# Kernel tuning notes

Hardware: AMD Instinct MI355X
Metric: run time of the kernel (lower is better)

Reference implementation:

```python
import jax, jax.numpy as jnp
import numpy as np

B, S = 256, 512
V, E, H, O = 256, 128, 256, 128


def setup_inputs() -> dict:
    key = jax.random.key(0)
    ks = jax.random.split(key, 8)
    s_e = 1.0 / np.sqrt(H)
    return {
        "x": jax.random.randint(ks[0], (B, S), 0, V),
        "emb": jax.random.normal(ks[1], (V, E), dtype=jnp.float32),
        "W_ih": jax.random.uniform(ks[2], (4 * H, E), jnp.float32, -s_e, s_e),
        "W_hh": jax.random.uniform(ks[3], (4 * H, H), jnp.float32, -s_e, s_e),
        "b_ih": jax.random.uniform(ks[4], (4 * H,), jnp.float32, -s_e, s_e),
        "b_hh": jax.random.uniform(ks[5], (4 * H,), jnp.float32, -s_e, s_e),
        "W_out": jax.random.uniform(ks[6], (O, H), jnp.float32, -s_e, s_e),
        "b_out": jax.random.uniform(ks[7], (O,), jnp.float32, -s_e, s_e),
    }


def _lstm_last_h(xe, W_ih, W_hh, b_ih, b_hh):
    # xe: [B, S, E]. Precompute input contribution to all gates: [S, B, 4H]
    pre = jnp.einsum("bse,ge->sbg", xe, W_ih) + (b_ih + b_hh)
    Bn = xe.shape[0]
    h0 = jnp.zeros((Bn, H), xe.dtype)
    c0 = jnp.zeros((Bn, H), xe.dtype)

    def step(carry, p):
        h, c = carry
        gates = p + h @ W_hh.T  # [B, 4H]
        i, f, g, o = jnp.split(gates, 4, axis=-1)  # PyTorch gate order i,f,g,o
        i = jax.nn.sigmoid(i)
        f = jax.nn.sigmoid(f)
        g = jnp.tanh(g)
        o = jax.nn.sigmoid(o)
        c = f * c + i * g
        h = o * jnp.tanh(c)
        return (h, c), None

    (h, _), _ = jax.lax.scan(step, (h0, c0), pre)
    return h  # [B, H] == lstm output at last timestep


def reference(x, emb, W_ih, W_hh, b_ih, b_hh, W_out, b_out):
    xe = emb[x]  # [B, S, E] embedding lookup
    h_last = _lstm_last_h(xe, W_ih, W_hh, b_ih, b_hh)
    return h_last @ W_out.T + b_out  # [B, O]
```

## Files before the change

kernel.cpp:

```cpp
#include <hip/hip_runtime.h>


typedef _Float16 f16x8 __attribute__((ext_vector_type(8)));
typedef _Float16 f16x4 __attribute__((ext_vector_type(4)));
typedef float    f32x4 __attribute__((ext_vector_type(4)));

#define B_  256
#define S_  512
#define V_  256
#define E_  128
#define H_  256
#define O_  128

#define T_OFF     0u
#define HLAST_OFF (512u << 10)
#define WPK_OFF   (768u << 10)

__global__ void build_table(const float* __restrict__ emb,
                            const float* __restrict__ W_ih,
                            const float* __restrict__ b_ih,
                            const float* __restrict__ b_hh,
                            _Float16* __restrict__ T2h) {
    const int v   = blockIdx.x;
    const int tid = threadIdx.x;

    __shared__ float e[E_];
    if (tid < E_) e[tid] = emb[v * E_ + tid];
    __syncthreads();

    f16x4 tv;
#pragma unroll
    for (int t = 0; t < 4; ++t) {
        const int g = t * 256 + tid;
        const float4* wp = (const float4*)(W_ih + g * E_);
        float acc = 0.f;
#pragma unroll
        for (int i = 0; i < E_ / 4; ++i) {
            float4 w = wp[i];
            acc += w.x * e[4*i] + w.y * e[4*i+1] + w.z * e[4*i+2] + w.w * e[4*i+3];
        }
        tv[t] = (_Float16)(acc + b_ih[g] + b_hh[g]);
    }
    *(f16x4*)(T2h + ((size_t)v * 256 + tid) * 4) = tv;
}

__global__ void prepack(const float* __restrict__ W_hh,
                        _Float16* __restrict__ Wpk) {
    const int blk = blockIdx.x;
    const int ktS = blk >> 3;
    const int j   = blk & 7;
    const int kt  = 6 + ktS;
    const int tid = threadIdx.x;
    const int wv = tid >> 6, l = tid & 63, l15 = l & 15, quad = l >> 4;
    const int n  = j * 128 + wv * 16 + l15;
    const int k0 = kt * 32 + quad * 8;
    const float4* wp = (const float4*)(W_hh + (size_t)n * H_ + k0);
    float4 w0 = wp[0];
    float4 w1 = wp[1];
    f16x8 f = (f16x8){
        (_Float16)w0.x, (_Float16)w0.y, (_Float16)w0.z, (_Float16)w0.w,
        (_Float16)w1.x, (_Float16)w1.y, (_Float16)w1.z, (_Float16)w1.w};
    *(f16x8*)(Wpk + ((size_t)blk * 512 + tid) * 8) = f;
}

__device__ __forceinline__ float sig_fast(float x) {
    float t = __builtin_amdgcn_exp2f(-1.4426950408889634f * x);
    return __builtin_amdgcn_rcpf(1.f + t);
}
__device__ __forceinline__ float tanh_fast(float x) {
    x = fminf(fmaxf(x, -30.f), 30.f);
    float t = __builtin_amdgcn_exp2f(-2.8853900817779268f * x);
    return (1.f - t) * __builtin_amdgcn_rcpf(1.f + t);
}

#define HSTRIDE 272

__launch_bounds__(512, 2)
__global__ void lstm_persistent(const int* __restrict__ x,
                                const float* __restrict__ W_hh,
                                const _Float16* __restrict__ T2h,
                                const _Float16* __restrict__ Wpk,
                                float* __restrict__ hlast) {
    const int tid    = threadIdx.x;
    const int wv     = tid >> 6;
    const int l      = tid & 63;
    const int l15    = l & 15;
    const int quad   = l >> 4;
    const int stripe = blockIdx.x;
    const int uu     = wv * 16 + l15;

    __shared__ __align__(16) _Float16 wlds[8][8][2][512];
    __shared__ __align__(16) _Float16 hbuf[2][4][HSTRIDE];
    __shared__ __align__(16) _Float16 zbuf[256];

    if (tid < 128) ((int*)zbuf)[tid] = 0;

    f16x8 wreg[8][4];
#pragma unroll
    for (int j = 0; j < 8; ++j) {
        const float* wr = W_hh + (size_t)(j * 128 + uu) * H_ + quad * 8;
#pragma unroll
        for (int kt = 0; kt < 6; ++kt) {
            const float4* wp = (const float4*)(wr + kt * 32);
            float4 w0 = wp[0];
            float4 w1 = wp[1];
            f16x8 f = (f16x8){
                (_Float16)w0.x, (_Float16)w0.y, (_Float16)w0.z, (_Float16)w0.w,
                (_Float16)w1.x, (_Float16)w1.y, (_Float16)w1.z, (_Float16)w1.w};
            if (kt < 2)
                *(f16x8*)&wlds[wv][j][kt][(size_t)l * 8] = f;
            else
                wreg[j][kt - 2] = f;
        }
    }

    const int grow = stripe * 4 + quad;
    float c2[2] = {0.f, 0.f};

    int xv = x[(size_t)grow * S_];

    __syncthreads();

    for (int s = 0; s < S_; ++s) {
        f16x4 tcv[2];
        tcv[0] = *(const f16x4*)(T2h + ((size_t)xv * 256 + uu) * 4);
        tcv[1] = *(const f16x4*)(T2h + ((size_t)xv * 256 + uu + 128) * 4);
        if (s + 1 < S_) xv = x[(size_t)grow * S_ + s + 1];

        f32x4 acc[8];
#pragma unroll
        for (int j = 0; j < 8; ++j) acc[j] = (f32x4){0.f, 0.f, 0.f, 0.f};

        if (s > 0) {
            const _Float16* ha = ((l15 & 3) == 0)
                ? (&hbuf[(s - 1) & 1][l15 >> 2][0] + quad * 8)
                : (zbuf + quad * 8);

#pragma unroll
            for (int pass = 0; pass < 2; ++pass) {
                f16x8 wstr[4][2];
#pragma unroll
                for (int jj = 0; jj < 4; ++jj)
#pragma unroll
                    for (int ktS = 0; ktS < 2; ++ktS)
                        wstr[jj][ktS] = *(const f16x8*)(
                            Wpk + ((size_t)((ktS * 8 + pass * 4 + jj) * 512 + tid)) * 8);

#pragma unroll
                for (int kt = 0; kt < 8; ++kt) {
                    f16x8 a = *(const f16x8*)(ha + kt * 32);
                    if (kt < 2) {
#pragma unroll
                        for (int jj = 0; jj < 4; ++jj) {
                            f16x8 b = *(const f16x8*)
                                &wlds[wv][pass * 4 + jj][kt][(size_t)l * 8];
                            acc[pass * 4 + jj] =
                                __builtin_amdgcn_mfma_f32_16x16x32_f16(
                                    a, b, acc[pass * 4 + jj], 0, 0, 0);
                        }
                    } else if (kt < 6) {
#pragma unroll
                        for (int jj = 0; jj < 4; ++jj)
                            acc[pass * 4 + jj] =
                                __builtin_amdgcn_mfma_f32_16x16x32_f16(
                                    a, wreg[pass * 4 + jj][kt - 2],
                                    acc[pass * 4 + jj], 0, 0, 0);
                    } else {
#pragma unroll
                        for (int jj = 0; jj < 4; ++jj)
                            acc[pass * 4 + jj] =
                                __builtin_amdgcn_mfma_f32_16x16x32_f16(
                                    a, wstr[jj][kt - 6],
                                    acc[pass * 4 + jj], 0, 0, 0);
                    }
                }
            }
        }

        const bool last = (s == S_ - 1);
#pragma unroll
        for (int p = 0; p < 2; ++p) {
            float gi = sig_fast (acc[0 + p][0] + (float)tcv[p][0]);
            float gf = sig_fast (acc[2 + p][0] + (float)tcv[p][1]);
            float gg = tanh_fast(acc[4 + p][0] + (float)tcv[p][2]);
            float go = sig_fast (acc[6 + p][0] + (float)tcv[p][3]);
            float cc = gf * c2[p] + gi * gg;
            c2[p] = cc;
            float hv = go * tanh_fast(cc);
            if (!last) {
                hbuf[s & 1][quad][uu + p * 128] = (_Float16)hv;
            } else {
                hlast[(size_t)grow * H_ + uu + p * 128] = hv;
            }
        }

        __syncthreads();
    }
}

__global__ void out_kernel(const float* __restrict__ hlast,
                           const float* __restrict__ W_out,
                           const float* __restrict__ b_out,
                           float* __restrict__ out) {
    const int b = blockIdx.x;
    const int o = threadIdx.x;
    __shared__ float hl[H_];
    hl[o]       = hlast[b * H_ + o];
    hl[o + 128] = hlast[b * H_ + o + 128];
    __syncthreads();
    const float4* wp = (const float4*)(W_out + o * H_);
    float acc = 0.f;
#pragma unroll
    for (int i = 0; i < H_ / 4; ++i) {
        float4 w = wp[i];
        acc += w.x * hl[4*i] + w.y * hl[4*i+1] + w.z * hl[4*i+2] + w.w * hl[4*i+3];
    }
    out[b * O_ + o] = acc + b_out[o];
}

extern "C" void kernel_launch(void* const* d_in, const int* in_sizes, int n_in,
                              void* d_out, int out_size, void* d_ws, size_t ws_size,
                              hipStream_t stream) {
    const int*   x     = (const int*)  d_in[0];
    const float* emb   = (const float*)d_in[1];
    const float* W_ih  = (const float*)d_in[2];
    const float* W_hh  = (const float*)d_in[3];
    const float* b_ih  = (const float*)d_in[4];
    const float* b_hh  = (const float*)d_in[5];
    const float* W_out = (const float*)d_in[6];
    const float* b_out = (const float*)d_in[7];
    float* out = (float*)d_out;

    char* ws = (char*)d_ws;
    _Float16* T2h   = (_Float16*)(ws + T_OFF);
    float*    hlast = (float*)(ws + HLAST_OFF);
    _Float16* Wpk   = (_Float16*)(ws + WPK_OFF);

    build_table<<<dim3(V_), dim3(256), 0, stream>>>(emb, W_ih, b_ih, b_hh, T2h);
    prepack<<<dim3(16), dim3(512), 0, stream>>>(W_hh, Wpk);
    lstm_persistent<<<dim3(64), dim3(512), 0, stream>>>(x, W_hh, T2h, Wpk, hlast);
    out_kernel<<<dim3(B_), dim3(O_), 0, stream>>>(hlast, W_out, b_out, out);
}
```

Measured before the change: 915.8 us.

## Split LSTM recurrence across 16 waves with one hidden-unit slice each

Doubles the persistent LSTM block from 512 to 1024 threads, so each wave computes the four gates for a single 16-unit slice instead of two. This halves the serial MFMA chain per wave on each time step. The W_hh split is rebalanced to two k-tiles in LDS, three in registers and three streamed from a repacked global buffer, with the streamed loads issued early inside the k-loop. The launch bound of (1024, 4) asks for more occupancy than a CU can hold and may tightly cap registers, which risks spills.

Result: slower. 1.162 ms (+26.9%).

```diff
diff --git a/kernel.cpp b/kernel.cpp
--- a/kernel.cpp
+++ b/kernel.cpp
@@ -47,12 +47,12 @@
 __global__ void prepack(const float* __restrict__ W_hh,
                         _Float16* __restrict__ Wpk) {
     const int blk = blockIdx.x;
-    const int ktS = blk >> 3;
-    const int j   = blk & 7;
-    const int kt  = 6 + ktS;
+    const int ktS = blk >> 2;
+    const int j   = blk & 3;
+    const int kt  = 5 + ktS;
     const int tid = threadIdx.x;
     const int wv = tid >> 6, l = tid & 63, l15 = l & 15, quad = l >> 4;
-    const int n  = j * 128 + wv * 16 + l15;
+    const int n  = j * 256 + wv * 16 + l15;
     const int k0 = kt * 32 + quad * 8;
     const float4* wp = (const float4*)(W_hh + (size_t)n * H_ + k0);
     float4 w0 = wp[0];
@@ -60,7 +60,7 @@
     f16x8 f = (f16x8){
         (_Float16)w0.x, (_Float16)w0.y, (_Float16)w0.z, (_Float16)w0.w,
         (_Float16)w1.x, (_Float16)w1.y, (_Float16)w1.z, (_Float16)w1.w};
-    *(f16x8*)(Wpk + ((size_t)blk * 512 + tid) * 8) = f;
+    *(f16x8*)(Wpk + ((size_t)blk * 1024 + tid) * 8) = f;
 }
 
 __device__ __forceinline__ float sig_fast(float x) {
@@ -75,7 +75,7 @@
 
 #define HSTRIDE 272
 
-__launch_bounds__(512, 2)
+__launch_bounds__(1024, 4)
 __global__ void lstm_persistent(const int* __restrict__ x,
                                 const float* __restrict__ W_hh,
                                 const _Float16* __restrict__ T2h,
@@ -89,18 +89,18 @@
     const int stripe = blockIdx.x;
     const int uu     = wv * 16 + l15;
 
-    __shared__ __align__(16) _Float16 wlds[8][8][2][512];
+    __shared__ __align__(16) _Float16 wlds[16][4][2][512];
     __shared__ __align__(16) _Float16 hbuf[2][4][HSTRIDE];
     __shared__ __align__(16) _Float16 zbuf[256];
 
     if (tid < 128) ((int*)zbuf)[tid] = 0;
 
-    f16x8 wreg[8][4];
-#pragma unroll
-    for (int j = 0; j < 8; ++j) {
-        const float* wr = W_hh + (size_t)(j * 128 + uu) * H_ + quad * 8;
-#pragma unroll
-        for (int kt = 0; kt < 6; ++kt) {
+    f16x8 wreg[4][3];
+#pragma unroll
+    for (int j = 0; j < 4; ++j) {
+        const float* wr = W_hh + (size_t)(j * 256 + uu) * H_ + quad * 8;
+#pragma unroll
+        for (int kt = 0; kt < 5; ++kt) {
             const float4* wp = (const float4*)(wr + kt * 32);
             float4 w0 = wp[0];
             float4 w1 = wp[1];
@@ -115,82 +115,89 @@
     }
 
     const int grow = stripe * 4 + quad;
-    float c2[2] = {0.f, 0.f};
+    float c1 = 0.f;
 
     int xv = x[(size_t)grow * S_];
 
     __syncthreads();
 
     for (int s = 0; s < S_; ++s) {
-        f16x4 tcv[2];
-        tcv[0] = *(const f16x4*)(T2h + ((size_t)xv * 256 + uu) * 4);
-        tcv[1] = *(const f16x4*)(T2h + ((size_t)xv * 256 + uu + 128) * 4);
+        f16x4 tcv = *(const f16x4*)(T2h + ((size_t)xv * 256 + uu) * 4);
         if (s + 1 < S_) xv = x[(size_t)grow * S_ + s + 1];
 
-        f32x4 acc[8];
-#pragma unroll
-        for (int j = 0; j < 8; ++j) acc[j] = (f32x4){0.f, 0.f, 0.f, 0.f};
+        f32x4 acc[4];
+#pragma unroll
+        for (int j = 0; j < 4; ++j) acc[j] = (f32x4){0.f, 0.f, 0.f, 0.f};
 
         if (s > 0) {
             const _Float16* ha = ((l15 & 3) == 0)
                 ? (&hbuf[(s - 1) & 1][l15 >> 2][0] + quad * 8)
                 : (zbuf + quad * 8);
 
-#pragma unroll
-            for (int pass = 0; pass < 2; ++pass) {
-                f16x8 wstr[4][2];
-#pragma unroll
-                for (int jj = 0; jj < 4; ++jj)
-#pragma unroll
-                    for (int ktS = 0; ktS < 2; ++ktS)
-                        wstr[jj][ktS] = *(const f16x8*)(
-                            Wpk + ((size_t)((ktS * 8 + pass * 4 + jj) * 512 + tid)) * 8);
-
-#pragma unroll
-                for (int kt = 0; kt < 8; ++kt) {
-                    f16x8 a = *(const f16x8*)(ha + kt * 32);
-                    if (kt < 2) {
-#pragma unroll
-                        for (int jj = 0; jj < 4; ++jj) {
-                            f16x8 b = *(const f16x8*)
-                                &wlds[wv][pass * 4 + jj][kt][(size_t)l * 8];
-                            acc[pass * 4 + jj] =
-                                __builtin_amdgcn_mfma_f32_16x16x32_f16(
-                                    a, b, acc[pass * 4 + jj], 0, 0, 0);
-                        }
-                    } else if (kt < 6) {
-#pragma unroll
-                        for (int jj = 0; jj < 4; ++jj)
-                            acc[pass * 4 + jj] =
-                                __builtin_amdgcn_mfma_f32_16x16x32_f16(
-                                    a, wreg[pass * 4 + jj][kt - 2],
-                                    acc[pass * 4 + jj], 0, 0, 0);
-                    } else {
-#pragma unroll
-                        for (int jj = 0; jj < 4; ++jj)
-                            acc[pass * 4 + jj] =
-                                __builtin_amdgcn_mfma_f32_16x16x32_f16(
-                                    a, wstr[jj][kt - 6],
-                                    acc[pass * 4 + jj], 0, 0, 0);
+            f16x8 wstA[4], wstB[4];
+#pragma unroll
+            for (int j = 0; j < 4; ++j)
+                wstA[j] = *(const f16x8*)(
+                    Wpk + ((size_t)((0 * 4 + j) * 1024 + tid)) * 8);
+
+#pragma unroll
+            for (int kt = 0; kt < 8; ++kt) {
+                f16x8 a = *(const f16x8*)(ha + kt * 32);
+                if (kt < 2) {
+#pragma unroll
+                    for (int j = 0; j < 4; ++j) {
+                        f16x8 b = *(const f16x8*)&wlds[wv][j][kt][(size_t)l * 8];
+                        acc[j] = __builtin_amdgcn_mfma_f32_16x16x32_f16(
+                            a, b, acc[j], 0, 0, 0);
                     }
+                } else if (kt < 5) {
+#pragma unroll
+                    for (int j = 0; j < 4; ++j)
+                        acc[j] = __builtin_amdgcn_mfma_f32_16x16x32_f16(
+                            a, wreg[j][kt - 2], acc[j], 0, 0, 0);
+                } else if (kt == 5) {
+#pragma unroll
+                    for (int j = 0; j < 4; ++j)
+                        acc[j] = __builtin_amdgcn_mfma_f32_16x16x32_f16(
+                            a, wstA[j], acc[j], 0, 0, 0);
+                } else if (kt == 6) {
+#pragma unroll
+                    for (int j = 0; j < 4; ++j)
+                        acc[j] = __builtin_amdgcn_mfma_f32_16x16x32_f16(
+                            a, wstB[j], acc[j], 0, 0, 0);
+                } else {
+#pragma unroll
+                    for (int j = 0; j < 4; ++j)
+                        acc[j] = __builtin_amdgcn_mfma_f32_16x16x32_f16(
+                            a, wstA[j], acc[j], 0, 0, 0);
+                }
+                if (kt == 4) {
+#pragma unroll
+                    for (int j = 0; j < 4; ++j)
+                        wstB[j] = *(const f16x8*)(
+                            Wpk + ((size_t)((1 * 4 + j) * 1024 + tid)) * 8);
+                } else if (kt == 5) {
+#pragma unroll
+                    for (int j = 0; j < 4; ++j)
+                        wstA[j] = *(const f16x8*)(
+                            Wpk + ((size_t)((2 * 4 + j) * 1024 + tid)) * 8);
                 }
             }
         }
 
         const bool last = (s == S_ - 1);
-#pragma unroll
-        for (int p = 0; p < 2; ++p) {
-            float gi = sig_fast (acc[0 + p][0] + (float)tcv[p][0]);
-            float gf = sig_fast (acc[2 + p][0] + (float)tcv[p][1]);
-            float gg = tanh_fast(acc[4 + p][0] + (float)tcv[p][2]);
-            float go = sig_fast (acc[6 + p][0] + (float)tcv[p][3]);
-            float cc = gf * c2[p] + gi * gg;
-            c2[p] = cc;
+        {
+            float gi = sig_fast (acc[0][0] + (float)tcv[0]);
+            float gf = sig_fast (acc[1][0] + (float)tcv[1]);
+            float gg = tanh_fast(acc[2][0] + (float)tcv[2]);
+            float go = sig_fast (acc[3][0] + (float)tcv[3]);
+            float cc = gf * c1 + gi * gg;
+            c1 = cc;
             float hv = go * tanh_fast(cc);
             if (!last) {
-                hbuf[s & 1][quad][uu + p * 128] = (_Float16)hv;
+                hbuf[s & 1][quad][uu] = (_Float16)hv;
             } else {
-                hlast[(size_t)grow * H_ + uu + p * 128] = hv;
+                hlast[(size_t)grow * H_ + uu] = hv;
             }
         }
 
@@ -237,7 +244,7 @@
     _Float16* Wpk   = (_Float16*)(ws + WPK_OFF);
 
     build_table<<<dim3(V_), dim3(256), 0, stream>>>(emb, W_ih, b_ih, b_hh, T2h);
-    prepack<<<dim3(16), dim3(512), 0, stream>>>(W_hh, Wpk);
-    lstm_persistent<<<dim3(64), dim3(512), 0, stream>>>(x, W_hh, T2h, Wpk, hlast);
+    prepack<<<dim3(12), dim3(1024), 0, stream>>>(W_hh, Wpk);
+    lstm_persistent<<<dim3(64), dim3(1024), 0, stream>>>(x, W_hh, T2h, Wpk, hlast);
     out_kernel<<<dim3(B_), dim3(O_), 0, stream>>>(hlast, W_out, b_out, out);
 }
```
